# Optimization experiments

Measured on AMD Instinct MI355X. Metric: run time of the kernel, lower is better.

Reference implementation:

```python
import jax, jax.numpy as jnp
import numpy as np

MUL = 128          # hidden multiplicity for both 0e and 1o
OUT_MUL = 16       # output multiplicity for 0e and 1o
INV_SQRT_MUL = 1.0 / np.sqrt(MUL).astype(np.float32)


def setup_inputs() -> dict:
    key = jax.random.key(0)
    k_x, k1s, k1v, k2s, k2v = jax.random.split(key, 5)
    N = 200000
    # node features: 128 scalars (0e) followed by 128 vectors (1o, 3 components each)
    x = jax.random.normal(k_x, (N, MUL + 3 * MUL), dtype=jnp.float32)
    # e3nn Linear weights are standard normal; path norm 1/sqrt(fan_in) applied in forward
    w1_s = jax.random.normal(k1s, (MUL, 2 * MUL), dtype=jnp.float32)  # 128x0e -> 256x0e (scalars + gates)
    w1_v = jax.random.normal(k1v, (MUL, MUL), dtype=jnp.float32)      # 128x1o -> 128x1o
    w2_s = jax.random.normal(k2s, (MUL, OUT_MUL), dtype=jnp.float32)  # 128x0e -> 16x0e
    w2_v = jax.random.normal(k2v, (MUL, OUT_MUL), dtype=jnp.float32)  # 128x1o -> 16x1o
    return {"x": x, "w1_s": w1_s, "w1_v": w1_v, "w2_s": w2_s, "w2_v": w2_v}


def reference(x, w1_s, w1_v, w2_s, w2_v):
    N = x.shape[0]
    s = x[:, :MUL]                                   # [N, 128] scalars 0e
    v = x[:, MUL:].reshape(N, MUL, 3)                # [N, 128, 3] vectors 1o

    # --- Linear 1: hidden -> 256x0e + 128x1o (block-diagonal per irrep) ---
    h_s = (s @ w1_s) * INV_SQRT_MUL                  # [N, 256]
    h_v = jnp.einsum('nmc,mk->nkc', v, w1_v) * INV_SQRT_MUL  # [N, 128, 3]

    # --- Gate: leading 128 scalars -> silu, trailing 128 scalars gate vectors ---
    act_s = jax.nn.silu(h_s[:, :MUL])                # [N, 128]
    gates = jax.nn.sigmoid(h_s[:, MUL:])             # [N, 128]
    gated_v = h_v * gates[:, :, None]                # [N, 128, 3]

    # --- Linear 2: 128x0e + 128x1o -> 16x0e + 16x1o ---
    out_s = (act_s @ w2_s) * INV_SQRT_MUL            # [N, 16]
    out_v = jnp.einsum('nmc,mk->nkc', gated_v, w2_v) * INV_SQRT_MUL  # [N, 16, 3]

    return jnp.concatenate([out_s, out_v.reshape(N, 3 * OUT_MUL)], axis=1)  # [N, 64]
```

## Files before the change

### kernel.cpp

```cpp
#include <hip/hip_runtime.h>

typedef short bx8 __attribute__((ext_vector_type(8)));
typedef unsigned short ux4 __attribute__((ext_vector_type(4)));
typedef float fx4 __attribute__((ext_vector_type(4)));

#define INV 0.08838834764831843f
#define LP 136
#define TR 32
#define NROWS 200000
#define NT (NROWS / TR)
#define NTHREADS 640
#define NBLOCKS 256

__device__ __forceinline__ unsigned short f2bf(float f) {
  unsigned u = __builtin_bit_cast(unsigned, f);
  u += 0x7FFFu + ((u >> 16) & 1u);
  return (unsigned short)(u >> 16);
}
__device__ __forceinline__ float bf2f(unsigned short h) {
  unsigned u = ((unsigned)h) << 16;
  return __builtin_bit_cast(float, u);
}
__device__ __forceinline__ float sigm(float z) { return 1.0f / (1.0f + __expf(-z)); }

__global__ __launch_bounds__(NTHREADS) void nlr_kernel(
    const float* __restrict__ x, const float* __restrict__ w1_s,
    const float* __restrict__ w1_v, const float* __restrict__ w2_s,
    const float* __restrict__ w2_v, float* __restrict__ out) {
  __shared__ short lds[5 * TR * LP];
  short* sS = lds;
  short* vS0 = lds + TR * LP;
  short* gS = lds + 4 * TR * LP;

  const int tid = threadIdx.x;
  const int w = tid >> 6;
  const int lane = tid & 63;
  const int quad = lane >> 4;
  const int c16 = lane & 15;
  const int mrow0 = quad * 8;

  bx8 Wf[4][4];
  if (w < 4) {
#pragma unroll
    for (int jjb = 0; jjb < 4; ++jjb) {
      const int col = (w * 4 + jjb) * 16 + c16;
#pragma unroll
      for (int kb = 0; kb < 4; ++kb) {
        bx8 f;
#pragma unroll
        for (int jj = 0; jj < 8; ++jj)
          f[jj] = (short)f2bf(w1_s[(kb * 32 + mrow0 + jj) * 256 + col]);
        Wf[jjb][kb] = f;
      }
    }
  } else {
    const int half = (w - 4) & 1;
#pragma unroll
    for (int jjb = 0; jjb < 4; ++jjb) {
      const int col = (half * 4 + jjb) * 16 + c16;
#pragma unroll
      for (int kb = 0; kb < 4; ++kb) {
        bx8 f;
#pragma unroll
        for (int jj = 0; jj < 8; ++jj)
          f[jj] = (short)f2bf(w1_v[(kb * 32 + mrow0 + jj) * 128 + col]);
        Wf[jjb][kb] = f;
      }
    }
  }
  bx8 W2f[4];
  {
    const float* w2 = ((w & 3) == 0) ? w2_s : w2_v;
#pragma unroll
    for (int kb = 0; kb < 4; ++kb) {
      bx8 f;
#pragma unroll
      for (int jj = 0; jj < 8; ++jj)
        f[jj] = (short)f2bf(w2[(kb * 32 + mrow0 + jj) * 16 + c16]);
      W2f[kb] = f;
    }
  }

  for (int tile = blockIdx.x; tile < NT; tile += gridDim.x) {
    const float* xb = x + (size_t)tile * (TR * 512);
    for (int t = tid; t < 2048; t += NTHREADS) {
      const int n = (t & 1023) >> 5;
      const int ch = t & 31;
      if (t < 1024) {
        const fx4 f = *(const fx4*)(xb + n * 512 + ch * 4);
        ux4 p = {f2bf(f[0]), f2bf(f[1]), f2bf(f[2]), f2bf(f[3])};
        *(ux4*)(sS + n * LP + ch * 4) = p;
      } else {
        const float* bp = xb + n * 512 + 128 + ch * 12;
        const fx4 a = *(const fx4*)bp;
        const fx4 b = *(const fx4*)(bp + 4);
        const fx4 c = *(const fx4*)(bp + 8);
        ux4 p0 = {f2bf(a[0]), f2bf(a[3]), f2bf(b[2]), f2bf(c[1])};
        ux4 p1 = {f2bf(a[1]), f2bf(b[0]), f2bf(b[3]), f2bf(c[2])};
        ux4 p2 = {f2bf(a[2]), f2bf(b[1]), f2bf(c[0]), f2bf(c[3])};
        *(ux4*)(vS0 + 0 * TR * LP + n * LP + ch * 4) = p0;
        *(ux4*)(vS0 + 1 * TR * LP + n * LP + ch * 4) = p1;
        *(ux4*)(vS0 + 2 * TR * LP + n * LP + ch * 4) = p2;
      }
    }
    __syncthreads();

    fx4 acc[4][2];
    {
      const short* src = (w < 4) ? sS : (vS0 + ((w - 4) >> 1) * TR * LP);
#pragma unroll
      for (int rb = 0; rb < 2; ++rb) {
        bx8 B[4];
        const int rbase = (rb * 16 + c16) * LP + quad * 8;
#pragma unroll
        for (int kb = 0; kb < 4; ++kb) B[kb] = *(const bx8*)(src + rbase + kb * 32);
#pragma unroll
        for (int jjb = 0; jjb < 4; ++jjb) {
          fx4 a = {0.f, 0.f, 0.f, 0.f};
#pragma unroll
          for (int kb = 0; kb < 4; ++kb)
            a = __builtin_amdgcn_mfma_f32_16x16x32_bf16(Wf[jjb][kb], B[kb], a, 0, 0, 0);
          acc[jjb][rb] = a;
        }
      }
    }
    if (w >= 2 && w < 4) {
#pragma unroll
      for (int rb = 0; rb < 2; ++rb)
#pragma unroll
        for (int jjb = 0; jjb < 4; ++jjb) {
          const int jb = w * 4 + jjb;
          ux4 p;
#pragma unroll
          for (int r = 0; r < 4; ++r) p[r] = f2bf(sigm(acc[jjb][rb][r] * INV));
          *(ux4*)(gS + (rb * 16 + c16) * LP + (jb - 8) * 16 + quad * 4) = p;
        }
    }
    __syncthreads();

    if (w < 2) {
#pragma unroll
      for (int rb = 0; rb < 2; ++rb)
#pragma unroll
        for (int jjb = 0; jjb < 4; ++jjb) {
          const int jb = w * 4 + jjb;
          ux4 p;
#pragma unroll
          for (int r = 0; r < 4; ++r) {
            const float h = acc[jjb][rb][r] * INV;
            p[r] = f2bf(h * sigm(h));
          }
          *(ux4*)(sS + (rb * 16 + c16) * LP + jb * 16 + quad * 4) = p;
        }
    } else if (w >= 4) {
      const int vc = (w - 4) >> 1, half = (w - 4) & 1;
      short* gv = vS0 + vc * TR * LP;
#pragma unroll
      for (int rb = 0; rb < 2; ++rb)
#pragma unroll
        for (int jjb = 0; jjb < 4; ++jjb) {
          const int jb = half * 4 + jjb;
          const ux4 g = *(const ux4*)(gS + (rb * 16 + c16) * LP + jb * 16 + quad * 4);
          ux4 p;
#pragma unroll
          for (int r = 0; r < 4; ++r)
            p[r] = f2bf(acc[jjb][rb][r] * INV * bf2f(g[r]));
          *(ux4*)(gv + (rb * 16 + c16) * LP + jb * 16 + quad * 4) = p;
        }
    }
    __syncthreads();

    if (w < 8) {
      const int g = w & 3, rb = w >> 2;
      const short* src = (g == 0) ? sS : (vS0 + (g - 1) * TR * LP);
      fx4 a = {0.f, 0.f, 0.f, 0.f};
      const int rbase = (rb * 16 + c16) * LP + quad * 8;
#pragma unroll
      for (int kb = 0; kb < 4; ++kb) {
        const bx8 B = *(const bx8*)(src + rbase + kb * 32);
        a = __builtin_amdgcn_mfma_f32_16x16x32_bf16(W2f[kb], B, a, 0, 0, 0);
      }
      const size_t n = (size_t)tile * TR + rb * 16 + c16;
      if (g == 0) {
        fx4 o = {a[0] * INV, a[1] * INV, a[2] * INV, a[3] * INV};
        *(fx4*)(out + n * 64 + quad * 4) = o;
      } else {
        const int c = g - 1;
#pragma unroll
        for (int r = 0; r < 4; ++r)
          out[n * 64 + 16 + 3 * (quad * 4 + r) + c] = a[r] * INV;
      }
    }
    __syncthreads();
  }
}

extern "C" void kernel_launch(void* const* d_in, const int* in_sizes, int n_in,
                              void* d_out, int out_size, void* d_ws, size_t ws_size,
                              hipStream_t stream) {
  const float* x    = (const float*)d_in[0];
  const float* w1_s = (const float*)d_in[1];
  const float* w1_v = (const float*)d_in[2];
  const float* w2_s = (const float*)d_in[3];
  const float* w2_v = (const float*)d_in[4];
  nlr_kernel<<<NBLOCKS, NTHREADS, 0, stream>>>(x, w1_s, w1_v, w2_s, w2_v, (float*)d_out);
}
```

Measured before the change: 634.5 us.

## Prefetch next tile into registers and split activation buffers to drop a barrier

Halves the per-iteration tile to 16 rows and issues the global loads for the next tile into registers right after the first barrier, so memory latency overlaps with the MFMA and gating work of the current tile. Activations get their own LDS region separate from the staged inputs, which removes the trailing barrier at the end of each loop iteration. The costs are more loop iterations with three barriers each over fewer rows, extra registers for the prefetch, and only 4 of 10 waves doing the second GEMM.

```diff
diff --git a/kernel.cpp b/kernel.cpp
--- a/kernel.cpp
+++ b/kernel.cpp
@@ -6,7 +6,7 @@
 
 #define INV 0.08838834764831843f
 #define LP 136
-#define TR 32
+#define TR 16
 #define NROWS 200000
 #define NT (NROWS / TR)
 #define NTHREADS 640
@@ -27,10 +27,10 @@
     const float* __restrict__ x, const float* __restrict__ w1_s,
     const float* __restrict__ w1_v, const float* __restrict__ w2_s,
     const float* __restrict__ w2_v, float* __restrict__ out) {
-  __shared__ short lds[5 * TR * LP];
-  short* sS = lds;
-  short* vS0 = lds + TR * LP;
-  short* gS = lds + 4 * TR * LP;
+  __shared__ short lds[9 * TR * LP];
+  short* X = lds;
+  short* ACT = lds + 4 * TR * LP;
+  short* GS = lds + 8 * TR * LP;
 
   const int tid = threadIdx.x;
   const int w = tid >> 6;
@@ -39,6 +39,12 @@
   const int c16 = lane & 15;
   const int mrow0 = quad * 8;
 
+  const bool hasS = tid < 512;
+  const bool hasV = (tid < 384) || (tid >= 512);
+  const int sn = tid >> 5, sch = tid & 31;
+  const int vu = (tid < 384) ? (tid + 128) : (tid - 512);
+  const int vn = vu >> 5, vch = vu & 31;
+
   bx8 Wf[4][4];
   if (w < 4) {
 #pragma unroll
@@ -70,7 +76,7 @@
   }
   bx8 W2f[4];
   {
-    const float* w2 = ((w & 3) == 0) ? w2_s : w2_v;
+    const float* w2 = (w == 0) ? w2_s : w2_v;
 #pragma unroll
     for (int kb = 0; kb < 4; ++kb) {
       bx8 f;
@@ -81,117 +87,120 @@
     }
   }
 
-  for (int tile = blockIdx.x; tile < NT; tile += gridDim.x) {
+  fx4 pf_s, pf_a, pf_b, pf_c;
+
+  int tile = blockIdx.x;
+  {
     const float* xb = x + (size_t)tile * (TR * 512);
-    for (int t = tid; t < 2048; t += NTHREADS) {
-      const int n = (t & 1023) >> 5;
-      const int ch = t & 31;
-      if (t < 1024) {
-        const fx4 f = *(const fx4*)(xb + n * 512 + ch * 4);
-        ux4 p = {f2bf(f[0]), f2bf(f[1]), f2bf(f[2]), f2bf(f[3])};
-        *(ux4*)(sS + n * LP + ch * 4) = p;
-      } else {
-        const float* bp = xb + n * 512 + 128 + ch * 12;
-        const fx4 a = *(const fx4*)bp;
-        const fx4 b = *(const fx4*)(bp + 4);
-        const fx4 c = *(const fx4*)(bp + 8);
-        ux4 p0 = {f2bf(a[0]), f2bf(a[3]), f2bf(b[2]), f2bf(c[1])};
-        ux4 p1 = {f2bf(a[1]), f2bf(b[0]), f2bf(b[3]), f2bf(c[2])};
-        ux4 p2 = {f2bf(a[2]), f2bf(b[1]), f2bf(c[0]), f2bf(c[3])};
-        *(ux4*)(vS0 + 0 * TR * LP + n * LP + ch * 4) = p0;
-        *(ux4*)(vS0 + 1 * TR * LP + n * LP + ch * 4) = p1;
-        *(ux4*)(vS0 + 2 * TR * LP + n * LP + ch * 4) = p2;
-      }
-    }
+    if (hasS) pf_s = *(const fx4*)(xb + sn * 512 + sch * 4);
+    if (hasV) {
+      const float* bp = xb + vn * 512 + 128 + vch * 12;
+      pf_a = *(const fx4*)bp; pf_b = *(const fx4*)(bp + 4); pf_c = *(const fx4*)(bp + 8);
+    }
+  }
+
+  while (tile < NT) {
+    if (hasS) {
+      ux4 p = {f2bf(pf_s[0]), f2bf(pf_s[1]), f2bf(pf_s[2]), f2bf(pf_s[3])};
+      *(ux4*)(X + sn * LP + sch * 4) = p;
+    }
+    if (hasV) {
+      ux4 p0 = {f2bf(pf_a[0]), f2bf(pf_a[3]), f2bf(pf_b[2]), f2bf(pf_c[1])};
+      ux4 p1 = {f2bf(pf_a[1]), f2bf(pf_b[0]), f2bf(pf_b[3]), f2bf(pf_c[2])};
+      ux4 p2 = {f2bf(pf_a[2]), f2bf(pf_b[1]), f2bf(pf_c[0]), f2bf(pf_c[3])};
+      *(ux4*)(X + 1 * TR * LP + vn * LP + vch * 4) = p0;
+      *(ux4*)(X + 2 * TR * LP + vn * LP + vch * 4) = p1;
+      *(ux4*)(X + 3 * TR * LP + vn * LP + vch * 4) = p2;
+    }
+    const int nxt = tile + NBLOCKS;
     __syncthreads();
 
-    fx4 acc[4][2];
+    if (nxt < NT) {
+      const float* xb = x + (size_t)nxt * (TR * 512);
+      if (hasS) pf_s = *(const fx4*)(xb + sn * 512 + sch * 4);
+      if (hasV) {
+        const float* bp = xb + vn * 512 + 128 + vch * 12;
+        pf_a = *(const fx4*)bp; pf_b = *(const fx4*)(bp + 4); pf_c = *(const fx4*)(bp + 8);
+      }
+    }
+
+    fx4 acc[4];
     {
-      const short* src = (w < 4) ? sS : (vS0 + ((w - 4) >> 1) * TR * LP);
-#pragma unroll
-      for (int rb = 0; rb < 2; ++rb) {
-        bx8 B[4];
-        const int rbase = (rb * 16 + c16) * LP + quad * 8;
-#pragma unroll
-        for (int kb = 0; kb < 4; ++kb) B[kb] = *(const bx8*)(src + rbase + kb * 32);
-#pragma unroll
-        for (int jjb = 0; jjb < 4; ++jjb) {
-          fx4 a = {0.f, 0.f, 0.f, 0.f};
-#pragma unroll
-          for (int kb = 0; kb < 4; ++kb)
-            a = __builtin_amdgcn_mfma_f32_16x16x32_bf16(Wf[jjb][kb], B[kb], a, 0, 0, 0);
-          acc[jjb][rb] = a;
+      const short* src = (w < 4) ? X : (X + (1 + ((w - 4) >> 1)) * TR * LP);
+      bx8 B[4];
+      const int rbase = c16 * LP + mrow0;
+#pragma unroll
+      for (int kb = 0; kb < 4; ++kb) B[kb] = *(const bx8*)(src + rbase + kb * 32);
+#pragma unroll
+      for (int jjb = 0; jjb < 4; ++jjb) {
+        fx4 a = {0.f, 0.f, 0.f, 0.f};
+#pragma unroll
+        for (int kb = 0; kb < 4; ++kb)
+          a = __builtin_amdgcn_mfma_f32_16x16x32_bf16(Wf[jjb][kb], B[kb], a, 0, 0, 0);
+        acc[jjb] = a;
+      }
+    }
+    if (w == 2 || w == 3) {
+#pragma unroll
+      for (int jjb = 0; jjb < 4; ++jjb) {
+        const int jb = w * 4 + jjb;
+        ux4 p;
+#pragma unroll
+        for (int r = 0; r < 4; ++r) p[r] = f2bf(sigm(acc[jjb][r] * INV));
+        *(ux4*)(GS + c16 * LP + (jb - 8) * 16 + quad * 4) = p;
+      }
+    }
+    __syncthreads();
+
+    if (w < 2) {
+#pragma unroll
+      for (int jjb = 0; jjb < 4; ++jjb) {
+        const int jb = w * 4 + jjb;
+        ux4 p;
+#pragma unroll
+        for (int r = 0; r < 4; ++r) {
+          const float h = acc[jjb][r] * INV;
+          p[r] = f2bf(h * sigm(h));
         }
-      }
-    }
-    if (w >= 2 && w < 4) {
-#pragma unroll
-      for (int rb = 0; rb < 2; ++rb)
-#pragma unroll
-        for (int jjb = 0; jjb < 4; ++jjb) {
-          const int jb = w * 4 + jjb;
-          ux4 p;
-#pragma unroll
-          for (int r = 0; r < 4; ++r) p[r] = f2bf(sigm(acc[jjb][rb][r] * INV));
-          *(ux4*)(gS + (rb * 16 + c16) * LP + (jb - 8) * 16 + quad * 4) = p;
-        }
-    }
-    __syncthreads();
-
-    if (w < 2) {
-#pragma unroll
-      for (int rb = 0; rb < 2; ++rb)
-#pragma unroll
-        for (int jjb = 0; jjb < 4; ++jjb) {
-          const int jb = w * 4 + jjb;
-          ux4 p;
-#pragma unroll
-          for (int r = 0; r < 4; ++r) {
-            const float h = acc[jjb][rb][r] * INV;
-            p[r] = f2bf(h * sigm(h));
-          }
-          *(ux4*)(sS + (rb * 16 + c16) * LP + jb * 16 + quad * 4) = p;
-        }
+        *(ux4*)(ACT + c16 * LP + jb * 16 + quad * 4) = p;
+      }
     } else if (w >= 4) {
       const int vc = (w - 4) >> 1, half = (w - 4) & 1;
-      short* gv = vS0 + vc * TR * LP;
-#pragma unroll
-      for (int rb = 0; rb < 2; ++rb)
-#pragma unroll
-        for (int jjb = 0; jjb < 4; ++jjb) {
-          const int jb = half * 4 + jjb;
-          const ux4 g = *(const ux4*)(gS + (rb * 16 + c16) * LP + jb * 16 + quad * 4);
-          ux4 p;
-#pragma unroll
-          for (int r = 0; r < 4; ++r)
-            p[r] = f2bf(acc[jjb][rb][r] * INV * bf2f(g[r]));
-          *(ux4*)(gv + (rb * 16 + c16) * LP + jb * 16 + quad * 4) = p;
-        }
+      short* gv = ACT + (1 + vc) * TR * LP;
+#pragma unroll
+      for (int jjb = 0; jjb < 4; ++jjb) {
+        const int jb = half * 4 + jjb;
+        const ux4 g = *(const ux4*)(GS + c16 * LP + jb * 16 + quad * 4);
+        ux4 p;
+#pragma unroll
+        for (int r = 0; r < 4; ++r)
+          p[r] = f2bf(acc[jjb][r] * INV * bf2f(g[r]));
+        *(ux4*)(gv + c16 * LP + jb * 16 + quad * 4) = p;
+      }
     }
     __syncthreads();
 
-    if (w < 8) {
-      const int g = w & 3, rb = w >> 2;
-      const short* src = (g == 0) ? sS : (vS0 + (g - 1) * TR * LP);
+    if (w < 4) {
+      const short* src = ACT + w * TR * LP;
       fx4 a = {0.f, 0.f, 0.f, 0.f};
-      const int rbase = (rb * 16 + c16) * LP + quad * 8;
+      const int rbase = c16 * LP + mrow0;
 #pragma unroll
       for (int kb = 0; kb < 4; ++kb) {
         const bx8 B = *(const bx8*)(src + rbase + kb * 32);
         a = __builtin_amdgcn_mfma_f32_16x16x32_bf16(W2f[kb], B, a, 0, 0, 0);
       }
-      const size_t n = (size_t)tile * TR + rb * 16 + c16;
-      if (g == 0) {
+      const size_t n = (size_t)tile * TR + c16;
+      if (w == 0) {
         fx4 o = {a[0] * INV, a[1] * INV, a[2] * INV, a[3] * INV};
         *(fx4*)(out + n * 64 + quad * 4) = o;
       } else {
-        const int c = g - 1;
+        const int c = w - 1;
 #pragma unroll
         for (int r = 0; r < 4; ++r)
           out[n * 64 + 16 + 3 * (quad * 4 + r) + c] = a[r] * INV;
       }
     }
-    __syncthreads();
+    tile = nxt;
   }
 }
 
```

Result: faster. 583.7 us (-8.0%).
